# Performance work log

Hardware: AMD Instinct MI355X
Metric: run time of the kernel (lower is better)

Reference implementation:

```python
import jax, jax.numpy as jnp
import numpy as np
from jax import lax

B, D, BOND, OUT = 16384, 784, 5, 10

def setup_inputs() -> dict:
    key = jax.random.key(0)
    k = jax.random.split(key, 6)
    x = jax.random.uniform(k[0], (B, D), dtype=jnp.float32)
    core_first = jax.random.normal(k[1], (1, 2, BOND), dtype=jnp.float32) * 0.1
    cores_mid = jax.random.normal(k[2], (D - 2, BOND, 2, BOND), dtype=jnp.float32) * 0.1
    core_last = jax.random.normal(k[3], (BOND, 2, 1), dtype=jnp.float32) * 0.1
    # xavier_uniform for fc.weight with fan_in=1, fan_out=OUT
    bound = float(np.sqrt(6.0 / (1 + OUT)))
    fc_w = jax.random.uniform(k[4], (OUT, 1), dtype=jnp.float32, minval=-bound, maxval=bound)
    fc_b = jnp.zeros((OUT,), dtype=jnp.float32)
    return {"x": x, "core_first": core_first, "cores_mid": cores_mid,
            "core_last": core_last, "fc_w": fc_w, "fc_b": fc_b}

def reference(x, core_first, cores_mid, core_last, fc_w, fc_b):
    # x: [B, D] -> feature map [B, D, 2] = stack(1-x, x)
    xs = jnp.stack([1.0 - x, x], axis=-1)            # [B, D, 2]
    # first core: (1, 2, bond) -> initial carry [B, bond]
    carry0 = jnp.einsum('bi,ir->br', xs[:, 0], core_first[0])  # [B, bond]
    # sequential tensor-train contraction over middle sites via scan
    xs_mid = jnp.moveaxis(xs[:, 1:-1], 1, 0)          # [D-2, B, 2]
    def step(carry, inp):
        xi, core = inp                                # xi: [B,2], core: [bond,2,bond]
        carry = jnp.einsum('bl,bi,lir->br', carry, xi, core)
        return carry, None
    carry, _ = lax.scan(step, carry0, (xs_mid, cores_mid))
    # last core: (bond, 2, 1) -> scalar per batch element
    vlast = jnp.einsum('bi,li->bl', xs[:, -1], core_last[:, :, 0])  # [B, bond]
    res = jnp.sum(carry * vlast, axis=-1, keepdims=True)            # [B, 1]
    out = res @ fc_w.T + fc_b                          # [B, OUT]
    return out
```

## Files before the change

### kernel.cpp

```cpp
#include <hip/hip_runtime.h>


typedef float v4f __attribute__((ext_vector_type(4)));
typedef float v2f __attribute__((ext_vector_type(2)));

constexpr int Bn     = 16384;
constexpr int Dn     = 784;
constexpr int NOUT   = 10;
constexpr int NPAIR  = 390;
constexpr int PFV    = 41;
constexpr int PMAT   = 22;
constexpr int BWD_P0 = 349;
constexpr int PAIR_F = 100;

__device__ __forceinline__ v4f splat4(float x) { v4f v = {x, x, x, x}; return v; }
__device__ __forceinline__ v4f fma4(v4f a, v4f b, v4f c) {
    return __builtin_elementwise_fma(a, b, c);
}

struct Frag { v4f r[5]; float c4[5]; };

__device__ __forceinline__ void matstepLM(const Frag& M, Frag& T,
                                          const float* __restrict__ s, v2f xc) {
    const float xa = xc[0], xb = xc[1], xab = xa * xb;
    const v4f va = splat4(xa), vb = splat4(xb), vp = splat4(xab);
    const v4f* s4 = (const v4f*)s;
#pragma unroll
    for (int l = 0; l < 5; ++l) {
        v4f crow = fma4(vp, s4[15 + l], fma4(vb, s4[10 + l], fma4(va, s4[5 + l], s4[l])));
        v4f cq = (l < 4) ? s4[20 + l] : s4[24];
        float c4l = fmaf(xab, cq[3], fmaf(xb, cq[2], fmaf(xa, cq[1], cq[0])));
#pragma unroll
        for (int i = 0; i < 5; ++i) {
            float mil = (l < 4) ? M.r[i][l] : M.c4[i];
            if (l == 0) {
                T.r[i]  = splat4(mil) * crow;
                T.c4[i] = mil * c4l;
            } else {
                T.r[i]  = fma4(splat4(mil), crow, T.r[i]);
                T.c4[i] = fmaf(mil, c4l, T.c4[i]);
            }
        }
    }
}

__device__ __forceinline__ void vecstepLM(v4f& cv, float& c4,
                                          const float* __restrict__ s, v2f xc) {
    const float xa = xc[0], xb = xc[1], xab = xa * xb;
    const v4f va = splat4(xa), vb = splat4(xb), vp = splat4(xab);
    const v4f* s4 = (const v4f*)s;
    v4f acc; float a4;
#pragma unroll
    for (int l = 0; l < 5; ++l) {
        v4f crow = fma4(vp, s4[15 + l], fma4(vb, s4[10 + l], fma4(va, s4[5 + l], s4[l])));
        v4f cq = (l < 4) ? s4[20 + l] : s4[24];
        float c4l = fmaf(xab, cq[3], fmaf(xb, cq[2], fmaf(xa, cq[1], cq[0])));
        float cl = (l < 4) ? cv[l] : c4;
        if (l == 0) { acc = splat4(cl) * crow; a4 = cl * c4l; }
        else        { acc = fma4(splat4(cl), crow, acc); a4 = fmaf(cl, c4l, a4); }
    }
    cv = acc; c4 = a4;
}

__global__ void prepack_pairs(const float* __restrict__ cm, float* __restrict__ pk)
{
    int idx = blockIdx.x * 256 + threadIdx.x;
    if (idx >= NPAIR * 100) return;
    int p = idx / 100, rest = idx - p * 100;
    int q = rest / 25, e = rest - q * 25;
    int l = e / 5, r = e - l * 5;
    int m1 = 2 * p + 1, m2 = 2 * p + 2;
    const float* L = cm + (size_t)(m1 * 5 + l) * 10;
    float acc = 0.f;
#pragma unroll
    for (int k = 0; k < 5; ++k) {
        float Lk = (q & 1) ? (L[5 + k] - L[k]) : L[k];
        const float* R = cm + (size_t)(m2 * 5 + k) * 10;
        float Rk = (q & 2) ? (R[5 + r] - R[r]) : R[r];
        acc = fmaf(Lk, Rk, acc);
    }
    int wl = l, wr = r;
    if (p >= BWD_P0) { wl = r; wr = l; }
    int off;
    if (wr < 4)      off = q * 20 + wl * 4 + wr;
    else if (wl < 4) off = 80 + wl * 4 + q;
    else             off = 96 + q;
    pk[(size_t)p * PAIR_F + off] = acc;
}

__global__ __launch_bounds__(1024, 4)
void mps_pair_kernel(const float* __restrict__ x,
                     const float* __restrict__ core_first,
                     const float* __restrict__ cores_mid,
                     const float* __restrict__ core_last,
                     const float* __restrict__ fc_w,
                     const float* __restrict__ fc_b,
                     const float* __restrict__ pk,
                     float* __restrict__ out)
{
    __shared__ float matbuf[7][25][64];
    __shared__ float bv[5][64];

    const int lane = threadIdx.x & 63;
    const int wave = threadIdx.x >> 6;
    const int wu   = __builtin_amdgcn_readfirstlane(wave);
    const int row  = blockIdx.x * 64 + lane;
    const float* __restrict__ xr = x + (size_t)row * Dn;
    const v2f* __restrict__ xr2 = (const v2f*)xr;

    if (wu >= 1 && wu <= 14) {
        const int p0 = PFV + PMAT * (wu - 1);

        Frag M, T;
        M.r[0] = {1,0,0,0}; M.r[1] = {0,1,0,0}; M.r[2] = {0,0,1,0};
        M.r[3] = {0,0,0,1}; M.r[4] = {0,0,0,0};
        M.c4[0] = 0; M.c4[1] = 0; M.c4[2] = 0; M.c4[3] = 0; M.c4[4] = 1;

        v2f x0 = xr2[p0 + 1], x1 = xr2[p0 + 2];
#pragma unroll 1
        for (int j = 0; j < PMAT; j += 2) {
            const float* s0 = pk + (size_t)(p0 + j) * PAIR_F;
            v2f nx0 = xr2[p0 + j + 3], nx1 = xr2[p0 + j + 4];
            matstepLM(M, T, s0, x0);
            matstepLM(T, M, s0 + PAIR_F, x1);
            x0 = nx0; x1 = nx1;
        }

        if (wu <= 7) {
#pragma unroll
            for (int i = 0; i < 5; ++i) {
#pragma unroll
                for (int r = 0; r < 4; ++r) matbuf[wu - 1][i * 5 + r][lane] = M.r[i][r];
                matbuf[wu - 1][i * 5 + 4][lane] = M.c4[i];
            }
        }
        __syncthreads();
        __syncthreads();
        if (wu >= 8) {
#pragma unroll
            for (int i = 0; i < 5; ++i) {
#pragma unroll
                for (int r = 0; r < 4; ++r) matbuf[wu - 8][i * 5 + r][lane] = M.r[i][r];
                matbuf[wu - 8][i * 5 + 4][lane] = M.c4[i];
            }
        }
        __syncthreads();
    } else if (wu == 0) {
        v2f x01 = xr2[0];
        float cl[5], cn[5];
#pragma unroll
        for (int r = 0; r < 5; ++r)
            cl[r] = fmaf(x01[0], core_first[5 + r] - core_first[r], core_first[r]);
        const float* cm0 = cores_mid;
#pragma unroll
        for (int r = 0; r < 5; ++r) {
            float a = 0.f;
#pragma unroll
            for (int l = 0; l < 5; ++l) {
                float m = fmaf(x01[1], cm0[l * 10 + 5 + r] - cm0[l * 10 + r], cm0[l * 10 + r]);
                a = fmaf(cl[l], m, a);
            }
            cn[r] = a;
        }
        v4f cv = {cn[0], cn[1], cn[2], cn[3]};
        float c4 = cn[4];

        v2f xc = xr2[1];
#pragma unroll 1
        for (int p = 0; p < PFV; ++p) {
            v2f nx = xr2[p + 2];
            vecstepLM(cv, c4, pk + (size_t)p * PAIR_F, xc);
            xc = nx;
        }
        cl[0] = cv[0]; cl[1] = cv[1]; cl[2] = cv[2]; cl[3] = cv[3]; cl[4] = c4;

        __syncthreads();
#pragma unroll 1
        for (int w2 = 0; w2 < 7; ++w2) {
            float v0[5];
#pragma unroll
            for (int r = 0; r < 5; ++r) v0[r] = cl[0] * matbuf[w2][r][lane];
#pragma unroll
            for (int l = 1; l < 5; ++l)
#pragma unroll
                for (int r = 0; r < 5; ++r)
                    v0[r] = fmaf(cl[l], matbuf[w2][l * 5 + r][lane], v0[r]);
#pragma unroll
            for (int r = 0; r < 5; ++r) cl[r] = v0[r];
        }
        __syncthreads();
        __syncthreads();
#pragma unroll 1
        for (int w2 = 0; w2 < 7; ++w2) {
            float v0[5];
#pragma unroll
            for (int r = 0; r < 5; ++r) v0[r] = cl[0] * matbuf[w2][r][lane];
#pragma unroll
            for (int l = 1; l < 5; ++l)
#pragma unroll
                for (int r = 0; r < 5; ++r)
                    v0[r] = fmaf(cl[l], matbuf[w2][l * 5 + r][lane], v0[r]);
#pragma unroll
            for (int r = 0; r < 5; ++r) cl[r] = v0[r];
        }
        float res = 0.f;
#pragma unroll
        for (int l = 0; l < 5; ++l) res = fmaf(cl[l], bv[l][lane], res);
        float* orow = out + (size_t)row * NOUT;
#pragma unroll
        for (int o = 0; o < NOUT; ++o) orow[o] = fmaf(res, fc_w[o], fc_b[o]);
    } else {
        v2f xz = xr2[391];
        float vl[5], vn[5];
#pragma unroll
        for (int l = 0; l < 5; ++l)
            vl[l] = fmaf(xz[1], core_last[2 * l + 1] - core_last[2 * l], core_last[2 * l]);
        const float* cmL = cores_mid + (size_t)781 * 50;
#pragma unroll
        for (int l = 0; l < 5; ++l) {
            float a = 0.f;
#pragma unroll
            for (int r = 0; r < 5; ++r) {
                float m = fmaf(xz[0], cmL[l * 10 + 5 + r] - cmL[l * 10 + r], cmL[l * 10 + r]);
                a = fmaf(m, vl[r], a);
            }
            vn[l] = a;
        }
        v4f cv = {vn[0], vn[1], vn[2], vn[3]};
        float c4 = vn[4];

        v2f xc = xr2[390];
#pragma unroll 1
        for (int p = 389; p >= BWD_P0; --p) {
            v2f nx = xr2[p];
            vecstepLM(cv, c4, pk + (size_t)p * PAIR_F, xc);
            xc = nx;
        }

        __syncthreads();
        __syncthreads();
        bv[0][lane] = cv[0]; bv[1][lane] = cv[1]; bv[2][lane] = cv[2];
        bv[3][lane] = cv[3]; bv[4][lane] = c4;
        __syncthreads();
    }
}

extern "C" void kernel_launch(void* const* d_in, const int* in_sizes, int n_in,
                              void* d_out, int out_size, void* d_ws, size_t ws_size,
                              hipStream_t stream) {
    const float* x          = (const float*)d_in[0];
    const float* core_first = (const float*)d_in[1];
    const float* cores_mid  = (const float*)d_in[2];
    const float* core_last  = (const float*)d_in[3];
    const float* fc_w       = (const float*)d_in[4];
    const float* fc_b       = (const float*)d_in[5];
    float* out              = (float*)d_out;
    float* pk               = (float*)d_ws;

    hipLaunchKernelGGL(prepack_pairs, dim3((NPAIR * 100 + 255) / 256), dim3(256),
                       0, stream, cores_mid, pk);
    hipLaunchKernelGGL(mps_pair_kernel, dim3(Bn / 64), dim3(1024), 0, stream,
                       x, core_first, cores_mid, core_last, fc_w, fc_b, pk, out);
}
```

Before: 125.0 us.

## Split each row's chain across two blocks and combine halves in finishing kernels

Each 64-row group is now handled by two blocks: one contracts the left half of the pair chain (a short vector prefix plus 15 matrix-product waves), the other contracts the right half (a backward vector suffix plus matrix waves applied to it). Each block writes a 5-wide boundary vector into the output buffer as scratch. Two small extra kernels then form the dot product and apply the fc layer. This doubles the block count and shortens each block's serial chain to improve latency and occupancy. The cost is two more launches, scratch traffic through global memory, and `res` sharing workspace with the prepacked cores, which it overwrites after they are used.

```diff
diff --git a/kernel.cpp b/kernel.cpp
--- a/kernel.cpp
+++ b/kernel.cpp
@@ -8,10 +8,12 @@
 constexpr int Dn     = 784;
 constexpr int NOUT   = 10;
 constexpr int NPAIR  = 390;
-constexpr int PFV    = 41;
-constexpr int PMAT   = 22;
-constexpr int BWD_P0 = 349;
+constexpr int PVEC   = 15;
+constexpr int PMAT   = 12;
+constexpr int RHP0   = 195;
+constexpr int BWD_P0 = 375;
 constexpr int PAIR_F = 100;
+constexpr int WROFF  = Bn * 5;
 
 __device__ __forceinline__ v4f splat4(float x) { v4f v = {x, x, x, x}; return v; }
 __device__ __forceinline__ v4f fma4(v4f a, v4f b, v4f c) {
@@ -88,28 +90,27 @@
     pk[(size_t)p * PAIR_F + off] = acc;
 }
 
-__global__ __launch_bounds__(1024, 4)
-void mps_pair_kernel(const float* __restrict__ x,
+__global__ __launch_bounds__(1024, 8)
+void mps_half_kernel(const float* __restrict__ x,
                      const float* __restrict__ core_first,
                      const float* __restrict__ cores_mid,
                      const float* __restrict__ core_last,
-                     const float* __restrict__ fc_w,
-                     const float* __restrict__ fc_b,
                      const float* __restrict__ pk,
                      float* __restrict__ out)
 {
-    __shared__ float matbuf[7][25][64];
-    __shared__ float bv[5][64];
+    __shared__ float matbuf[8][25][64];
 
     const int lane = threadIdx.x & 63;
     const int wave = threadIdx.x >> 6;
     const int wu   = __builtin_amdgcn_readfirstlane(wave);
-    const int row  = blockIdx.x * 64 + lane;
+    const int g    = blockIdx.x >> 1;
+    const int h    = blockIdx.x & 1;
+    const int row  = g * 64 + lane;
     const float* __restrict__ xr = x + (size_t)row * Dn;
     const v2f* __restrict__ xr2 = (const v2f*)xr;
 
-    if (wu >= 1 && wu <= 14) {
-        const int p0 = PFV + PMAT * (wu - 1);
+    if (wu >= 1) {
+        const int p0 = (h == 0 ? PVEC : RHP0) + PMAT * (wu - 1);
 
         Frag M, T;
         M.r[0] = {1,0,0,0}; M.r[1] = {0,1,0,0}; M.r[2] = {0,0,1,0};
@@ -126,26 +127,29 @@
             x0 = nx0; x1 = nx1;
         }
 
-        if (wu <= 7) {
+        const bool ph1 = (h == 0) ? (wu <= 8) : (wu >= 8);
+        const int  k   = (h == 0) ? (ph1 ? wu - 1 : wu - 9)
+                                  : (ph1 ? 15 - wu : 7 - wu);
+        if (ph1) {
 #pragma unroll
             for (int i = 0; i < 5; ++i) {
 #pragma unroll
-                for (int r = 0; r < 4; ++r) matbuf[wu - 1][i * 5 + r][lane] = M.r[i][r];
-                matbuf[wu - 1][i * 5 + 4][lane] = M.c4[i];
-            }
-        }
-        __syncthreads();
-        __syncthreads();
-        if (wu >= 8) {
+                for (int r = 0; r < 4; ++r) matbuf[k][i * 5 + r][lane] = M.r[i][r];
+                matbuf[k][i * 5 + 4][lane] = M.c4[i];
+            }
+        }
+        __syncthreads();
+        __syncthreads();
+        if (!ph1) {
 #pragma unroll
             for (int i = 0; i < 5; ++i) {
 #pragma unroll
-                for (int r = 0; r < 4; ++r) matbuf[wu - 8][i * 5 + r][lane] = M.r[i][r];
-                matbuf[wu - 8][i * 5 + 4][lane] = M.c4[i];
-            }
-        }
-        __syncthreads();
-    } else if (wu == 0) {
+                for (int r = 0; r < 4; ++r) matbuf[k][i * 5 + r][lane] = M.r[i][r];
+                matbuf[k][i * 5 + 4][lane] = M.c4[i];
+            }
+        }
+        __syncthreads();
+    } else if (h == 0) {
         v2f x01 = xr2[0];
         float cl[5], cn[5];
 #pragma unroll
@@ -167,7 +171,7 @@
 
         v2f xc = xr2[1];
 #pragma unroll 1
-        for (int p = 0; p < PFV; ++p) {
+        for (int p = 0; p < PVEC; ++p) {
             v2f nx = xr2[p + 2];
             vecstepLM(cv, c4, pk + (size_t)p * PAIR_F, xc);
             xc = nx;
@@ -176,39 +180,36 @@
 
         __syncthreads();
 #pragma unroll 1
-        for (int w2 = 0; w2 < 7; ++w2) {
+        for (int k = 0; k < 8; ++k) {
             float v0[5];
 #pragma unroll
-            for (int r = 0; r < 5; ++r) v0[r] = cl[0] * matbuf[w2][r][lane];
+            for (int r = 0; r < 5; ++r) v0[r] = cl[0] * matbuf[k][r][lane];
 #pragma unroll
             for (int l = 1; l < 5; ++l)
 #pragma unroll
                 for (int r = 0; r < 5; ++r)
-                    v0[r] = fmaf(cl[l], matbuf[w2][l * 5 + r][lane], v0[r]);
+                    v0[r] = fmaf(cl[l], matbuf[k][l * 5 + r][lane], v0[r]);
 #pragma unroll
             for (int r = 0; r < 5; ++r) cl[r] = v0[r];
         }
         __syncthreads();
         __syncthreads();
 #pragma unroll 1
-        for (int w2 = 0; w2 < 7; ++w2) {
+        for (int k = 0; k < 7; ++k) {
             float v0[5];
 #pragma unroll
-            for (int r = 0; r < 5; ++r) v0[r] = cl[0] * matbuf[w2][r][lane];
+            for (int r = 0; r < 5; ++r) v0[r] = cl[0] * matbuf[k][r][lane];
 #pragma unroll
             for (int l = 1; l < 5; ++l)
 #pragma unroll
                 for (int r = 0; r < 5; ++r)
-                    v0[r] = fmaf(cl[l], matbuf[w2][l * 5 + r][lane], v0[r]);
+                    v0[r] = fmaf(cl[l], matbuf[k][l * 5 + r][lane], v0[r]);
 #pragma unroll
             for (int r = 0; r < 5; ++r) cl[r] = v0[r];
         }
-        float res = 0.f;
-#pragma unroll
-        for (int l = 0; l < 5; ++l) res = fmaf(cl[l], bv[l][lane], res);
-        float* orow = out + (size_t)row * NOUT;
-#pragma unroll
-        for (int o = 0; o < NOUT; ++o) orow[o] = fmaf(res, fc_w[o], fc_b[o]);
+        float* o = out + (size_t)row * 5;
+#pragma unroll
+        for (int i = 0; i < 5; ++i) o[i] = cl[i];
     } else {
         v2f xz = xr2[391];
         float vl[5], vn[5];
@@ -236,13 +237,66 @@
             vecstepLM(cv, c4, pk + (size_t)p * PAIR_F, xc);
             xc = nx;
         }
-
-        __syncthreads();
-        __syncthreads();
-        bv[0][lane] = cv[0]; bv[1][lane] = cv[1]; bv[2][lane] = cv[2];
-        bv[3][lane] = cv[3]; bv[4][lane] = c4;
-        __syncthreads();
+        float u[5] = {cv[0], cv[1], cv[2], cv[3], c4};
+
+        __syncthreads();
+#pragma unroll 1
+        for (int k = 0; k < 8; ++k) {
+            float v0[5];
+#pragma unroll
+            for (int i = 0; i < 5; ++i) {
+                float a = matbuf[k][i * 5][lane] * u[0];
+#pragma unroll
+                for (int l = 1; l < 5; ++l)
+                    a = fmaf(matbuf[k][i * 5 + l][lane], u[l], a);
+                v0[i] = a;
+            }
+#pragma unroll
+            for (int i = 0; i < 5; ++i) u[i] = v0[i];
+        }
+        __syncthreads();
+        __syncthreads();
+#pragma unroll 1
+        for (int k = 0; k < 7; ++k) {
+            float v0[5];
+#pragma unroll
+            for (int i = 0; i < 5; ++i) {
+                float a = matbuf[k][i * 5][lane] * u[0];
+#pragma unroll
+                for (int l = 1; l < 5; ++l)
+                    a = fmaf(matbuf[k][i * 5 + l][lane], u[l], a);
+                v0[i] = a;
+            }
+#pragma unroll
+            for (int i = 0; i < 5; ++i) u[i] = v0[i];
+        }
+        float* o = out + WROFF + (size_t)row * 5;
+#pragma unroll
+        for (int i = 0; i < 5; ++i) o[i] = u[i];
     }
+}
+
+__global__ __launch_bounds__(256)
+void finish_dot(const float* __restrict__ outF, float* __restrict__ res)
+{
+    int r = blockIdx.x * 256 + threadIdx.x;
+    const float* vl = outF + (size_t)r * 5;
+    const float* wr = outF + WROFF + (size_t)r * 5;
+    float s = vl[0] * wr[0];
+#pragma unroll
+    for (int i = 1; i < 5; ++i) s = fmaf(vl[i], wr[i], s);
+    res[r] = s;
+}
+
+__global__ __launch_bounds__(256)
+void finish_out(const float* __restrict__ res, const float* __restrict__ fc_w,
+                const float* __restrict__ fc_b, float* __restrict__ out)
+{
+    int r = blockIdx.x * 256 + threadIdx.x;
+    float rv = res[r];
+    float* o = out + (size_t)r * NOUT;
+#pragma unroll
+    for (int j = 0; j < NOUT; ++j) o[j] = fmaf(rv, fc_w[j], fc_b[j]);
 }
 
 extern "C" void kernel_launch(void* const* d_in, const int* in_sizes, int n_in,
@@ -256,9 +310,14 @@
     const float* fc_b       = (const float*)d_in[5];
     float* out              = (float*)d_out;
     float* pk               = (float*)d_ws;
+    float* res              = (float*)d_ws;
 
     hipLaunchKernelGGL(prepack_pairs, dim3((NPAIR * 100 + 255) / 256), dim3(256),
                        0, stream, cores_mid, pk);
-    hipLaunchKernelGGL(mps_pair_kernel, dim3(Bn / 64), dim3(1024), 0, stream,
-                       x, core_first, cores_mid, core_last, fc_w, fc_b, pk, out);
-}
+    hipLaunchKernelGGL(mps_half_kernel, dim3(512), dim3(1024), 0, stream,
+                       x, core_first, cores_mid, core_last, pk, out);
+    hipLaunchKernelGGL(finish_dot, dim3(Bn / 256), dim3(256), 0, stream,
+                       out, res);
+    hipLaunchKernelGGL(finish_out, dim3(Bn / 256), dim3(256), 0, stream,
+                       res, fc_w, fc_b, out);
+}
```

New measurement: 266.2 us. 113% more time.

## Split chain into 8 waves with longer segments and final combine in backward wave

Applied to the files above, without the earlier changes.

The block shrinks from 16 to 8 waves: a forward vector wave covers 75 pairs, six matrix waves cover 40 pairs each, and a backward vector wave covers 75 pairs. The two-phase matbuf handoff with double __syncthreads is replaced by a single barrier, and the final combine moves into the backward wave, which multiplies its vector through the six matrices right to left. Fewer waves per row means fewer costly 5x5 matrix steps and less shared-memory combine work. The cost is a longer serial dependency chain per wave, which may limit latency hiding.

```diff
diff --git a/kernel.cpp b/kernel.cpp
--- a/kernel.cpp
+++ b/kernel.cpp
@@ -8,10 +8,10 @@
 constexpr int Dn     = 784;
 constexpr int NOUT   = 10;
 constexpr int NPAIR  = 390;
-constexpr int PFV    = 41;
-constexpr int PMAT   = 22;
-constexpr int BWD_P0 = 349;
 constexpr int PAIR_F = 100;
+constexpr int LV     = 75;
+constexpr int LM     = 40;
+constexpr int BWD0   = 315;
 
 __device__ __forceinline__ v4f splat4(float x) { v4f v = {x, x, x, x}; return v; }
 __device__ __forceinline__ v4f fma4(v4f a, v4f b, v4f c) {
@@ -62,7 +62,8 @@
     cv = acc; c4 = a4;
 }
 
-__global__ void prepack_pairs(const float* __restrict__ cm, float* __restrict__ pk)
+__global__ void prepack_pairs(const float* __restrict__ cm, float* __restrict__ pk,
+                              int bwd0)
 {
     int idx = blockIdx.x * 256 + threadIdx.x;
     if (idx >= NPAIR * 100) return;
@@ -80,7 +81,7 @@
         acc = fmaf(Lk, Rk, acc);
     }
     int wl = l, wr = r;
-    if (p >= BWD_P0) { wl = r; wr = l; }
+    if (p >= bwd0) { wl = r; wr = l; }
     int off;
     if (wr < 4)      off = q * 20 + wl * 4 + wr;
     else if (wl < 4) off = 80 + wl * 4 + q;
@@ -88,28 +89,27 @@
     pk[(size_t)p * PAIR_F + off] = acc;
 }
 
-__global__ __launch_bounds__(1024, 4)
-void mps_pair_kernel(const float* __restrict__ x,
-                     const float* __restrict__ core_first,
-                     const float* __restrict__ cores_mid,
-                     const float* __restrict__ core_last,
-                     const float* __restrict__ fc_w,
-                     const float* __restrict__ fc_b,
-                     const float* __restrict__ pk,
-                     float* __restrict__ out)
+__global__ __launch_bounds__(512, 2)
+void mps_seg_kernel(const float* __restrict__ x,
+                    const float* __restrict__ core_first,
+                    const float* __restrict__ cores_mid,
+                    const float* __restrict__ core_last,
+                    const float* __restrict__ fc_w,
+                    const float* __restrict__ fc_b,
+                    const float* __restrict__ pk,
+                    float* __restrict__ out)
 {
-    __shared__ float matbuf[7][25][64];
-    __shared__ float bv[5][64];
+    __shared__ float matbuf[6][25][64];
+    __shared__ float vbuf[5][64];
 
     const int lane = threadIdx.x & 63;
     const int wave = threadIdx.x >> 6;
     const int wu   = __builtin_amdgcn_readfirstlane(wave);
     const int row  = blockIdx.x * 64 + lane;
-    const float* __restrict__ xr = x + (size_t)row * Dn;
-    const v2f* __restrict__ xr2 = (const v2f*)xr;
-
-    if (wu >= 1 && wu <= 14) {
-        const int p0 = PFV + PMAT * (wu - 1);
+    const v2f* __restrict__ xr2 = (const v2f*)(x + (size_t)row * Dn);
+
+    if (wu >= 1 && wu <= 6) {
+        const int p0 = LV + LM * (wu - 1);
 
         Frag M, T;
         M.r[0] = {1,0,0,0}; M.r[1] = {0,1,0,0}; M.r[2] = {0,0,1,0};
@@ -118,7 +118,7 @@
 
         v2f x0 = xr2[p0 + 1], x1 = xr2[p0 + 2];
 #pragma unroll 1
-        for (int j = 0; j < PMAT; j += 2) {
+        for (int j = 0; j < LM; j += 2) {
             const float* s0 = pk + (size_t)(p0 + j) * PAIR_F;
             v2f nx0 = xr2[p0 + j + 3], nx1 = xr2[p0 + j + 4];
             matstepLM(M, T, s0, x0);
@@ -126,23 +126,12 @@
             x0 = nx0; x1 = nx1;
         }
 
-        if (wu <= 7) {
-#pragma unroll
-            for (int i = 0; i < 5; ++i) {
-#pragma unroll
-                for (int r = 0; r < 4; ++r) matbuf[wu - 1][i * 5 + r][lane] = M.r[i][r];
-                matbuf[wu - 1][i * 5 + 4][lane] = M.c4[i];
-            }
-        }
-        __syncthreads();
-        __syncthreads();
-        if (wu >= 8) {
-#pragma unroll
-            for (int i = 0; i < 5; ++i) {
-#pragma unroll
-                for (int r = 0; r < 4; ++r) matbuf[wu - 8][i * 5 + r][lane] = M.r[i][r];
-                matbuf[wu - 8][i * 5 + 4][lane] = M.c4[i];
-            }
+        const int k = wu - 1;
+#pragma unroll
+        for (int i = 0; i < 5; ++i) {
+#pragma unroll
+            for (int r = 0; r < 4; ++r) matbuf[k][i * 5 + r][lane] = M.r[i][r];
+            matbuf[k][i * 5 + 4][lane] = M.c4[i];
         }
         __syncthreads();
     } else if (wu == 0) {
@@ -167,48 +156,14 @@
 
         v2f xc = xr2[1];
 #pragma unroll 1
-        for (int p = 0; p < PFV; ++p) {
+        for (int p = 0; p < LV; ++p) {
             v2f nx = xr2[p + 2];
             vecstepLM(cv, c4, pk + (size_t)p * PAIR_F, xc);
             xc = nx;
         }
-        cl[0] = cv[0]; cl[1] = cv[1]; cl[2] = cv[2]; cl[3] = cv[3]; cl[4] = c4;
-
+        vbuf[0][lane] = cv[0]; vbuf[1][lane] = cv[1]; vbuf[2][lane] = cv[2];
+        vbuf[3][lane] = cv[3]; vbuf[4][lane] = c4;
         __syncthreads();
-#pragma unroll 1
-        for (int w2 = 0; w2 < 7; ++w2) {
-            float v0[5];
-#pragma unroll
-            for (int r = 0; r < 5; ++r) v0[r] = cl[0] * matbuf[w2][r][lane];
-#pragma unroll
-            for (int l = 1; l < 5; ++l)
-#pragma unroll
-                for (int r = 0; r < 5; ++r)
-                    v0[r] = fmaf(cl[l], matbuf[w2][l * 5 + r][lane], v0[r]);
-#pragma unroll
-            for (int r = 0; r < 5; ++r) cl[r] = v0[r];
-        }
-        __syncthreads();
-        __syncthreads();
-#pragma unroll 1
-        for (int w2 = 0; w2 < 7; ++w2) {
-            float v0[5];
-#pragma unroll
-            for (int r = 0; r < 5; ++r) v0[r] = cl[0] * matbuf[w2][r][lane];
-#pragma unroll
-            for (int l = 1; l < 5; ++l)
-#pragma unroll
-                for (int r = 0; r < 5; ++r)
-                    v0[r] = fmaf(cl[l], matbuf[w2][l * 5 + r][lane], v0[r]);
-#pragma unroll
-            for (int r = 0; r < 5; ++r) cl[r] = v0[r];
-        }
-        float res = 0.f;
-#pragma unroll
-        for (int l = 0; l < 5; ++l) res = fmaf(cl[l], bv[l][lane], res);
-        float* orow = out + (size_t)row * NOUT;
-#pragma unroll
-        for (int o = 0; o < NOUT; ++o) orow[o] = fmaf(res, fc_w[o], fc_b[o]);
     } else {
         v2f xz = xr2[391];
         float vl[5], vn[5];
@@ -231,17 +186,35 @@
 
         v2f xc = xr2[390];
 #pragma unroll 1
-        for (int p = 389; p >= BWD_P0; --p) {
+        for (int p = 389; p >= BWD0; --p) {
             v2f nx = xr2[p];
             vecstepLM(cv, c4, pk + (size_t)p * PAIR_F, xc);
             xc = nx;
         }
+        float u[5] = {cv[0], cv[1], cv[2], cv[3], c4};
 
         __syncthreads();
-        __syncthreads();
-        bv[0][lane] = cv[0]; bv[1][lane] = cv[1]; bv[2][lane] = cv[2];
-        bv[3][lane] = cv[3]; bv[4][lane] = c4;
-        __syncthreads();
+
+#pragma unroll 1
+        for (int k = 5; k >= 0; --k) {
+            float v0[5];
+#pragma unroll
+            for (int i = 0; i < 5; ++i) {
+                float a = matbuf[k][i * 5][lane] * u[0];
+#pragma unroll
+                for (int l = 1; l < 5; ++l)
+                    a = fmaf(matbuf[k][i * 5 + l][lane], u[l], a);
+                v0[i] = a;
+            }
+#pragma unroll
+            for (int i = 0; i < 5; ++i) u[i] = v0[i];
+        }
+        float res = 0.f;
+#pragma unroll
+        for (int l = 0; l < 5; ++l) res = fmaf(vbuf[l][lane], u[l], res);
+        float* orow = out + (size_t)row * NOUT;
+#pragma unroll
+        for (int o = 0; o < NOUT; ++o) orow[o] = fmaf(res, fc_w[o], fc_b[o]);
     }
 }
 
@@ -258,7 +231,7 @@
     float* pk               = (float*)d_ws;
 
     hipLaunchKernelGGL(prepack_pairs, dim3((NPAIR * 100 + 255) / 256), dim3(256),
-                       0, stream, cores_mid, pk);
-    hipLaunchKernelGGL(mps_pair_kernel, dim3(Bn / 64), dim3(1024), 0, stream,
+                       0, stream, cores_mid, pk, BWD0);
+    hipLaunchKernelGGL(mps_seg_kernel, dim3(Bn / 64), dim3(512), 0, stream,
                        x, core_first, cores_mid, core_last, fc_w, fc_b, pk, out);
 }
```

New measurement: 132.0 us. 5.6% more time.
